# Optimization experiments

Measured on AMD Instinct MI355X. Metric: run time of the kernel, lower is better.

Reference implementation:

```python
import jax, jax.numpy as jnp
import numpy as np

B, G, K, H, NC = 128, 12000, 512, 64, 100
FP = 2048
ALPHA = 0.1
STEPS = 10

def setup_inputs() -> dict:
    key = jax.random.key(0)
    ks = jax.random.split(key, 10)
    ctl = jax.random.normal(ks[0], (B, G), jnp.float32)
    # drug targets: sparse binary indicator per gene
    drug_targets = (jax.random.uniform(ks[1], (B, G)) < 0.01).astype(jnp.float32)
    cell_idx = jax.random.randint(ks[2], (B,), 0, NC, dtype=jnp.int32)
    drug_fp = jax.random.normal(ks[3], (B, FP), jnp.float32)  # unused in forward
    # gene->module membership (sparse-ish binary), ensure each module non-empty via deg clamp in model
    M = (jax.random.uniform(ks[4], (G, K)) < 0.02).astype(jnp.float32)
    # row-stochastic module adjacency for stable diffusion
    Araw = jax.random.uniform(ks[5], (K, K), jnp.float32)
    A = Araw / jnp.sum(Araw, axis=1, keepdims=True)
    W_in = jax.random.normal(ks[6], (2, H), jnp.float32) * 0.5
    b_in = jnp.zeros((H,), jnp.float32)
    cell_emb = jax.random.normal(ks[7], (NC, H), jnp.float32) * 0.02
    W_out = jax.random.normal(ks[8], (H, 1), jnp.float32) * 0.1
    b_out = jnp.zeros((1,), jnp.float32)
    return {"ctl": ctl, "drug_targets": drug_targets, "cell_idx": cell_idx,
            "drug_fp": drug_fp, "M": M, "A": A, "W_in": W_in, "b_in": b_in,
            "cell_emb": cell_emb, "W_out": W_out, "b_out": b_out}

def reference(ctl, drug_targets, cell_idx, drug_fp, M, A, W_in, b_in, cell_emb, W_out, b_out):
    # module degree (clamped) as in __init__
    mod_deg = jnp.maximum(jnp.sum(M, axis=0), 1.0)            # [K]
    x_gene = jnp.stack([ctl, drug_targets], axis=-1)          # [B,G,2]
    x_mod = jnp.einsum('gk,bgh->bkh', M, x_gene) / mod_deg[None, :, None]  # [B,K,2]
    S = jax.nn.relu(x_mod @ W_in + b_in)                      # [B,K,H]
    # 10-step personalized-PageRank-style diffusion over modules
    def step(Z, _):
        Z = (1.0 - ALPHA) * jnp.einsum('bkh,kl->blh', Z, A) + ALPHA * S
        return Z, None
    Z, _ = jax.lax.scan(step, S, None, length=STEPS)          # [B,K,H]
    h_gene = jnp.einsum('gk,bkh->bgh', M, Z)                  # [B,G,H]
    h_gene = h_gene + cell_emb[cell_idx][:, None, :]          # add cell embedding
    y = (h_gene @ W_out + b_out)[..., 0]                      # [B,G]
    return y
```

## Files before the change

### kernel.cpp

```cpp
#include <hip/hip_runtime.h>

#define B_    128
#define G_    12000
#define GP    12288
#define K_    512
#define H_    64
#define NSEG  12
#define SEGG  1024
#define BKT   64

typedef __attribute__((ext_vector_type(8))) short bf16x8;
typedef __attribute__((ext_vector_type(4))) float f32x4;

__device__ __forceinline__ unsigned short f2bf(float x) {
    union { float f; unsigned u; } v; v.f = x;
    unsigned r = (v.u + 0x7FFFu + ((v.u >> 16) & 1u)) >> 16;
    return (unsigned short)r;
}
__device__ __forceinline__ float bf2f(unsigned short b) {
    union { float f; unsigned u; } v; v.u = ((unsigned)b) << 16;
    return v.f;
}

__device__ __forceinline__ void mm_body(int k0, int l0, float* __restrict__ sm,
        const float* __restrict__ Aop, const float* __restrict__ Bop,
        const float* __restrict__ Cop, const float* __restrict__ Dop,
        float alpha, float beta, float* __restrict__ O, float* __restrict__ O2) {
    float (*Xa)[68] = (float(*)[68])sm;
    float (*Xb)[36] = (float(*)[36])(sm + 2176);
    int tid = threadIdx.x;
    int kg = tid & 15, lg = tid >> 4;
    float acc[2][2] = {};
    for (int jj = 0; jj < K_; jj += 64) {
#pragma unroll
        for (int i = 0; i < 2; ++i) {
            int lin = tid + i * 256;
            int r = lin >> 4, c4 = lin & 15;
            *(float4*)&Xa[r][c4 * 4] =
                *(const float4*)&Aop[(size_t)(l0 + r) * K_ + jj + c4 * 4];
        }
#pragma unroll
        for (int i = 0; i < 2; ++i) {
            int lin = tid + i * 256;
            int r = lin >> 3, c4 = lin & 7;
            *(float4*)&Xb[r][c4 * 4] =
                *(const float4*)&Bop[(size_t)(jj + r) * K_ + k0 + c4 * 4];
        }
        __syncthreads();
#pragma unroll 8
        for (int j = 0; j < 64; ++j) {
            float xa0 = Xa[lg * 2][j], xa1 = Xa[lg * 2 + 1][j];
            float xb0 = Xb[j][kg * 2], xb1 = Xb[j][kg * 2 + 1];
            acc[0][0] = fmaf(xa0, xb0, acc[0][0]);
            acc[0][1] = fmaf(xa0, xb1, acc[0][1]);
            acc[1][0] = fmaf(xa1, xb0, acc[1][0]);
            acc[1][1] = fmaf(xa1, xb1, acc[1][1]);
        }
        __syncthreads();
    }
#pragma unroll
    for (int i = 0; i < 2; ++i) {
        size_t idx = (size_t)(l0 + lg * 2 + i) * K_ + k0 + kg * 2;
        float2 v;
        v.x = alpha * acc[i][0];
        v.y = alpha * acc[i][1];
        if (beta != 0.0f) {
            float2 cc = *(const float2*)&Cop[idx];
            v.x = fmaf(beta, cc.x, v.x);
            v.y = fmaf(beta, cc.y, v.y);
        }
        *(float2*)&O[idx] = v;
        if (O2) {
            float2 dd = *(const float2*)&Dop[idx];
            float2 w2; w2.x = v.x + dd.x; w2.y = v.y + dd.y;
            *(float2*)&O2[idx] = w2;
        }
    }
}

__global__ __launch_bounds__(256) void k_pre(
        const float* __restrict__ ctl, const float* __restrict__ dt,
        const float* __restrict__ M, const float* __restrict__ A,
        const int* __restrict__ cidx, const float* __restrict__ cemb,
        const float* __restrict__ W_out, const float* __restrict__ b_out,
        unsigned short* __restrict__ XpT, unsigned short* __restrict__ MTb,
        unsigned short* __restrict__ Mb,
        float* __restrict__ AT, float* __restrict__ U2,
        float* __restrict__ cvec) {
    __shared__ float t[32][33];
    int bid = blockIdx.x, tid = threadIdx.x;
    if (bid < 3072) {
        int p = bid / 12, chunk = bid % 12;
        int ch = p >> 7, b = p & 127;
        const float* src = (ch ? dt : ctl) + (size_t)b * G_;
        int g = chunk * 1024 + tid * 4;
        float x0 = 0.f, x1 = 0.f, x2 = 0.f, x3 = 0.f;
        if (g + 3 < G_) {
            float4 v = *(const float4*)&src[g];
            x0 = v.x; x1 = v.y; x2 = v.z; x3 = v.w;
        } else {
            if (g + 0 < G_) x0 = src[g + 0];
            if (g + 1 < G_) x1 = src[g + 1];
            if (g + 2 < G_) x2 = src[g + 2];
            if (g + 3 < G_) x3 = src[g + 3];
        }
        unsigned short h0 = f2bf(x0), h1 = f2bf(x1), h2 = f2bf(x2), h3 = f2bf(x3);
        ushort4 hv; hv.x = h0; hv.y = h1; hv.z = h2; hv.w = h3;
        *(ushort4*)&XpT[(size_t)p * GP + g] = hv;
        ushort4 lv;
        lv.x = f2bf(x0 - bf2f(h0)); lv.y = f2bf(x1 - bf2f(h1));
        lv.z = f2bf(x2 - bf2f(h2)); lv.w = f2bf(x3 - bf2f(h3));
        *(ushort4*)&XpT[(size_t)(p + 256) * GP + g] = lv;
    } else if (bid < 9216) {
        int id = bid - 3072;
        int gt = id % 384, kt = id / 384;
        int g0 = gt * 32, k0 = kt * 32;
        int tx = tid & 31, ty = tid >> 5;
#pragma unroll
        for (int j = 0; j < 4; ++j) {
            int g = g0 + ty + 8 * j;
            float v = (g < G_) ? M[(size_t)g * K_ + k0 + tx] : 0.0f;
            t[ty + 8 * j][tx] = v;
            Mb[(size_t)g * K_ + k0 + tx] = f2bf(v);
        }
        __syncthreads();
#pragma unroll
        for (int j = 0; j < 4; ++j)
            MTb[(size_t)(k0 + ty + 8 * j) * GP + g0 + tx] = f2bf(t[tx][ty + 8 * j]);
    } else if (bid < 9472) {
        int id = bid - 9216;
        int x0 = (id & 15) * 32, y0 = (id >> 4) * 32;
        int tx = tid & 31, ty = tid >> 5;
#pragma unroll
        for (int j = 0; j < 4; ++j)
            t[ty + 8 * j][tx] = A[(size_t)(y0 + ty + 8 * j) * K_ + x0 + tx];
        __syncthreads();
#pragma unroll
        for (int j = 0; j < 4; ++j) {
            int row = x0 + ty + 8 * j, col = y0 + tx;
            float v = t[tx][ty + 8 * j];
            AT[(size_t)row * K_ + col] = v;
            U2[(size_t)row * K_ + col] = 0.09f * v + (row == col ? 0.1f : 0.0f);
        }
    } else {
        if (tid < B_) {
            int ci = cidx[tid];
            float acc = b_out[0];
#pragma unroll 8
            for (int h = 0; h < H_; ++h)
                acc = fmaf(cemb[ci * H_ + h], W_out[h], acc);
            cvec[tid] = acc;
        }
    }
}

__global__ __launch_bounds__(256) void k_gemm(
        const unsigned short* __restrict__ MTb, const unsigned short* __restrict__ XpT,
        float* __restrict__ Cp,
        const float* __restrict__ AT, const float* __restrict__ U2,
        float* __restrict__ M2, float* __restrict__ Yop) {
    __shared__ __align__(16) char smraw[36864];
    int bid = blockIdx.x, tid = threadIdx.x;
    if (bid < 192) {
        unsigned short (*Al)[72] = (unsigned short(*)[72])smraw;
        unsigned short (*Bl)[72] = (unsigned short(*)[72])(smraw + 18432);
        int tile = bid & 15, seg = bid >> 4;
        int m0 = (tile & 3) * 128, n0 = (tile >> 2) * 128;
        size_t gbase = (size_t)seg * SEGG;
        int wid = tid >> 6, lane = tid & 63;
        int wm = (wid >> 1) * 64, wn = (wid & 1) * 64;
        int r16 = lane & 15, kg8 = (lane >> 4) * 8;
        int ld_row = tid >> 3, ld_c8 = (tid & 7) * 8;
        f32x4 acc[4][4] = {};
        for (int kk = 0; kk < SEGG; kk += BKT) {
#pragma unroll
            for (int i = 0; i < 4; ++i) {
                int r = ld_row + 32 * i;
                *(uint4*)&Al[r][ld_c8] =
                    *(const uint4*)&MTb[(size_t)(m0 + r) * GP + gbase + kk + ld_c8];
                *(uint4*)&Bl[r][ld_c8] =
                    *(const uint4*)&XpT[(size_t)(n0 + r) * GP + gbase + kk + ld_c8];
            }
            __syncthreads();
#pragma unroll
            for (int ks = 0; ks < 2; ++ks) {
                bf16x8 af[4], bf[4];
#pragma unroll
                for (int mi = 0; mi < 4; ++mi)
                    af[mi] = *(const bf16x8*)&Al[wm + mi * 16 + r16][ks * 32 + kg8];
#pragma unroll
                for (int ni = 0; ni < 4; ++ni)
                    bf[ni] = *(const bf16x8*)&Bl[wn + ni * 16 + r16][ks * 32 + kg8];
#pragma unroll
                for (int mi = 0; mi < 4; ++mi)
#pragma unroll
                    for (int ni = 0; ni < 4; ++ni)
                        acc[mi][ni] = __builtin_amdgcn_mfma_f32_16x16x32_bf16(
                            af[mi], bf[ni], acc[mi][ni], 0, 0, 0);
            }
            __syncthreads();
        }
        float* C = Cp + (size_t)seg * (K_ * K_);
        int cr = (lane >> 4) * 4, cc = lane & 15;
#pragma unroll
        for (int mi = 0; mi < 4; ++mi)
#pragma unroll
            for (int ni = 0; ni < 4; ++ni) {
                size_t rb = (size_t)(m0 + wm + mi * 16 + cr) * K_
                          + (n0 + wn + ni * 16 + cc);
#pragma unroll
                for (int r = 0; r < 4; ++r)
                    C[rb + (size_t)r * K_] = acc[mi][ni][r];
            }
    } else {
        int id = bid - 192;
        mm_body((id & 15) * 32, (id >> 4) * 32, (float*)smraw,
                AT, AT, nullptr, U2, 0.81f, 0.0f, M2, Yop);
    }
}

__global__ __launch_bounds__(256) void k_red(
        const float* __restrict__ Cp, const unsigned short* __restrict__ MTb,
        const float* __restrict__ W_in, const float* __restrict__ b_in,
        const float* __restrict__ W_out, float* __restrict__ sout,
        const float* __restrict__ M2, const float* __restrict__ U2,
        float* __restrict__ M4, float* __restrict__ U4) {
    __shared__ __align__(16) float sm[4480];
    int bid = blockIdx.x, tid = threadIdx.x;
    if (bid < 256) {
        int kloc = tid >> 7, b = tid & 127;
        int k = bid * 2 + kloc;
        int cnt = 0;
        const unsigned short* mrow = MTb + (size_t)k * GP;
#pragma unroll
        for (int i = 0; i < 12; ++i) {
            uint4 v = *(const uint4*)&mrow[i * 1024 + b * 8];
            cnt += ((v.x & 0xFFFFu) != 0) + ((v.x >> 16) != 0);
            cnt += ((v.y & 0xFFFFu) != 0) + ((v.y >> 16) != 0);
            cnt += ((v.z & 0xFFFFu) != 0) + ((v.z >> 16) != 0);
            cnt += ((v.w & 0xFFFFu) != 0) + ((v.w >> 16) != 0);
        }
#pragma unroll
        for (int off = 32; off; off >>= 1) cnt += __shfl_down(cnt, off, 64);
        __shared__ int dsum[4];
        __shared__ float degs[2];
        int wv = tid >> 6;
        if ((tid & 63) == 0) dsum[wv] = cnt;
        __syncthreads();
        if (tid < 2) degs[tid] = (float)(dsum[tid * 2] + dsum[tid * 2 + 1]);
        __syncthreads();
        float x0 = 0.f, x1 = 0.f;
        for (int s = 0; s < NSEG; ++s) {
            const float* Cb = Cp + (size_t)s * (K_ * K_) + (size_t)k * K_;
            x0 += Cb[b]       + Cb[256 + b];
            x1 += Cb[128 + b] + Cb[384 + b];
        }
        float inv = 1.0f / fmaxf(degs[kloc], 1.0f);
        x0 *= inv; x1 *= inv;
        float s = 0.f;
#pragma unroll 8
        for (int h = 0; h < H_; ++h) {
            float v = fmaf(x0, W_in[h], fmaf(x1, W_in[H_ + h], b_in[h]));
            v = fmaxf(v, 0.f);
            s = fmaf(v, W_out[h], s);
        }
        sout[k * B_ + b] = s;
    } else {
        int id = bid - 256;
        int t = id & 255;
        if (id < 256)
            mm_body((t & 15) * 32, (t >> 4) * 32, sm, M2, M2, nullptr, nullptr,
                    1.0f, 0.0f, M4, nullptr);
        else
            mm_body((t & 15) * 32, (t >> 4) * 32, sm, M2, U2, U2, nullptr,
                    1.0f, 1.0f, U4, nullptr);
    }
}

__global__ __launch_bounds__(256) void k_p3(
        const float* __restrict__ M4, const float* __restrict__ U4,
        float* __restrict__ M8, float* __restrict__ U8,
        const float* __restrict__ Yop, const float* __restrict__ sout,
        float* __restrict__ q) {
    __shared__ __align__(16) float sm[4480];
    int bid = blockIdx.x, tid = threadIdx.x;
    if (bid < 512) {
        int t = bid & 255;
        if (bid < 256)
            mm_body((t & 15) * 32, (t >> 4) * 32, sm, M4, M4, nullptr, nullptr,
                    1.0f, 0.0f, M8, nullptr);
        else
            mm_body((t & 15) * 32, (t >> 4) * 32, sm, M4, U4, U4, nullptr,
                    1.0f, 1.0f, U8, nullptr);
    } else {
        int l = bid - 512;
        float* Wr  = sm;
        float* red = sm + 512;
        if (tid < 128)
            ((float4*)Wr)[tid] = ((const float4*)&Yop[(size_t)l * K_])[tid];
        __syncthreads();
        int b = tid & 127, seg = tid >> 7;
        int kb = seg * 256;
        float a0 = 0.f, a1 = 0.f, a2 = 0.f, a3 = 0.f;
#pragma unroll 4
        for (int kk = 0; kk < 256; kk += 4) {
            int k = kb + kk;
            a0 = fmaf(Wr[k + 0], sout[(k + 0) * B_ + b], a0);
            a1 = fmaf(Wr[k + 1], sout[(k + 1) * B_ + b], a1);
            a2 = fmaf(Wr[k + 2], sout[(k + 2) * B_ + b], a2);
            a3 = fmaf(Wr[k + 3], sout[(k + 3) * B_ + b], a3);
        }
        red[seg * 128 + b] = (a0 + a1) + (a2 + a3);
        __syncthreads();
        if (tid < 128)
            q[l * B_ + b] = red[b] + red[128 + b];
    }
}

__global__ __launch_bounds__(1024) void k_zfin(
        const float* __restrict__ M8, const float* __restrict__ U8,
        const float* __restrict__ q, const float* __restrict__ sout,
        unsigned short* __restrict__ zbT) {
    __shared__ __align__(16) float Wr[4 * K_];
    __shared__ float red[8][2][128];
    int tid = threadIdx.x;
    int l0 = blockIdx.x * 2;
    if (tid < 256)
        ((float4*)Wr)[tid] = ((const float4*)&M8[(size_t)l0 * K_])[tid];
    else if (tid < 512)
        ((float4*)&Wr[2 * K_])[tid - 256] =
            ((const float4*)&U8[(size_t)l0 * K_])[tid - 256];
    __syncthreads();
    int b = tid & 127, seg = tid >> 7;
    int kb = seg * 64;
    float a0m = 0.f, a0u = 0.f, a1m = 0.f, a1u = 0.f;
#pragma unroll 8
    for (int kk = 0; kk < 64; ++kk) {
        int k = kb + kk;
        float qv = q[k * B_ + b];
        float sv = sout[k * B_ + b];
        a0m = fmaf(Wr[k], qv, a0m);
        a0u = fmaf(Wr[2 * K_ + k], sv, a0u);
        a1m = fmaf(Wr[K_ + k], qv, a1m);
        a1u = fmaf(Wr[3 * K_ + k], sv, a1u);
    }
    red[seg][0][b] = a0m + a0u;
    red[seg][1][b] = a1m + a1u;
    __syncthreads();
    if (tid < 256) {
        int row = tid >> 7, bb = tid & 127;
        float t = 0.f;
#pragma unroll
        for (int u = 0; u < 8; ++u) t += red[u][row][bb];
        unsigned short hi = f2bf(t);
        unsigned short lo = f2bf(t - bf2f(hi));
        zbT[(size_t)bb * (2 * K_) + (l0 + row)]      = hi;
        zbT[(size_t)bb * (2 * K_) + K_ + (l0 + row)] = lo;
    }
}

__global__ __launch_bounds__(256) void k_yg(
        const unsigned short* __restrict__ Mb, const unsigned short* __restrict__ zbT,
        const float* __restrict__ cvec, float* __restrict__ y) {
    __shared__ __align__(16) unsigned short Al[128][72];
    __shared__ __align__(16) unsigned short Bh[128][72];
    __shared__ __align__(16) unsigned short Bl2[128][72];
    int tid = threadIdx.x;
    int g0 = blockIdx.x * 128;
    int wid = tid >> 6, lane = tid & 63;
    int wm = (wid >> 1) * 64, wn = (wid & 1) * 64;
    int r16 = lane & 15, kg8 = (lane >> 4) * 8;
    int ld_row = tid >> 3, ld_c8 = (tid & 7) * 8;
    f32x4 acc[4][4] = {};
    for (int kk = 0; kk < K_; kk += BKT) {
#pragma unroll
        for (int i = 0; i < 4; ++i) {
            int r = ld_row + 32 * i;
            *(uint4*)&Al[r][ld_c8] =
                *(const uint4*)&Mb[(size_t)(g0 + r) * K_ + kk + ld_c8];
            *(uint4*)&Bh[r][ld_c8] =
                *(const uint4*)&zbT[(size_t)r * (2 * K_) + kk + ld_c8];
            *(uint4*)&Bl2[r][ld_c8] =
                *(const uint4*)&zbT[(size_t)r * (2 * K_) + K_ + kk + ld_c8];
        }
        __syncthreads();
#pragma unroll
        for (int ks = 0; ks < 2; ++ks) {
            bf16x8 af[4], bh[4], bl[4];
#pragma unroll
            for (int mi = 0; mi < 4; ++mi)
                af[mi] = *(const bf16x8*)&Al[wm + mi * 16 + r16][ks * 32 + kg8];
#pragma unroll
            for (int ni = 0; ni < 4; ++ni) {
                bh[ni] = *(const bf16x8*)&Bh[wn + ni * 16 + r16][ks * 32 + kg8];
                bl[ni] = *(const bf16x8*)&Bl2[wn + ni * 16 + r16][ks * 32 + kg8];
            }
#pragma unroll
            for (int mi = 0; mi < 4; ++mi)
#pragma unroll
                for (int ni = 0; ni < 4; ++ni) {
                    acc[mi][ni] = __builtin_amdgcn_mfma_f32_16x16x32_bf16(
                        af[mi], bh[ni], acc[mi][ni], 0, 0, 0);
                    acc[mi][ni] = __builtin_amdgcn_mfma_f32_16x16x32_bf16(
                        af[mi], bl[ni], acc[mi][ni], 0, 0, 0);
                }
        }
        __syncthreads();
    }
    int cr = (lane >> 4) * 4, cc = lane & 15;
#pragma unroll
    for (int ni = 0; ni < 4; ++ni) {
        int b = wn + ni * 16 + cc;
        float cv = cvec[b];
#pragma unroll
        for (int mi = 0; mi < 4; ++mi) {
            int g = g0 + wm + mi * 16 + cr;
            if (g < G_) {
                float4 o;
                o.x = acc[mi][ni][0] + cv;
                o.y = acc[mi][ni][1] + cv;
                o.z = acc[mi][ni][2] + cv;
                o.w = acc[mi][ni][3] + cv;
                *(float4*)&y[(size_t)b * G_ + g] = o;
            }
        }
    }
}

extern "C" void kernel_launch(void* const* d_in, const int* in_sizes, int n_in,
                              void* d_out, int out_size, void* d_ws, size_t ws_size,
                              hipStream_t stream) {
    const float* ctl   = (const float*)d_in[0];
    const float* dt    = (const float*)d_in[1];
    const int*   cidx  = (const int*)d_in[2];
    const float* M     = (const float*)d_in[4];
    const float* A     = (const float*)d_in[5];
    const float* W_in  = (const float*)d_in[6];
    const float* b_in  = (const float*)d_in[7];
    const float* cemb  = (const float*)d_in[8];
    const float* W_out = (const float*)d_in[9];
    const float* b_out = (const float*)d_in[10];
    float* y = (float*)d_out;

    char* ws = (char*)d_ws;
    size_t o = 0;
    auto take = [&](size_t bytes) { char* p = ws + o; o = (o + bytes + 255) & ~(size_t)255; return p; };
    unsigned short* XpT = (unsigned short*)take((size_t)512 * GP * 2);
    unsigned short* MTb = (unsigned short*)take((size_t)K_ * GP * 2);
    unsigned short* Mb  = (unsigned short*)take((size_t)GP * K_ * 2);
    unsigned short* zbT = (unsigned short*)take((size_t)B_ * 2 * K_ * 2);
    float* Cp   = (float*)take((size_t)NSEG * K_ * K_ * 4);
    float* cvec = (float*)take(B_ * 4);
    float* AT   = (float*)take((size_t)K_ * K_ * 4);
    float* U2   = (float*)take((size_t)K_ * K_ * 4);
    float* M2   = (float*)take((size_t)K_ * K_ * 4);
    float* Yop  = (float*)take((size_t)K_ * K_ * 4);
    float* M4   = (float*)take((size_t)K_ * K_ * 4);
    float* U4   = (float*)take((size_t)K_ * K_ * 4);
    float* M8   = (float*)take((size_t)K_ * K_ * 4);
    float* U8   = (float*)take((size_t)K_ * K_ * 4);
    float* sout = (float*)take((size_t)K_ * B_ * 4);
    float* q    = (float*)take((size_t)K_ * B_ * 4);
    (void)ws_size; (void)in_sizes; (void)n_in; (void)out_size;

    k_pre<<<9473, 256, 0, stream>>>(ctl, dt, M, A, cidx, cemb, W_out, b_out,
                                    XpT, MTb, Mb, AT, U2, cvec);
    k_gemm<<<448, 256, 0, stream>>>(MTb, XpT, Cp, AT, U2, M2, Yop);
    k_red<<<768, 256, 0, stream>>>(Cp, MTb, W_in, b_in, W_out, sout,
                                   M2, U2, M4, U4);
    k_p3<<<1024, 256, 0, stream>>>(M4, U4, M8, U8, Yop, sout, q);
    k_zfin<<<K_ / 2, 1024, 0, stream>>>(M8, U8, q, sout, zbT);
    k_yg<<<(G_ + 127) / 128, 256, 0, stream>>>(Mb, zbT, cvec, y);
}
```

Measured before the change: 110.8 us.

## Drop bf16 lo-residual split of inputs and fuse module degree count into transpose

Result: no change. 112.9 us (+1.8%).

```diff
diff --git a/kernel.cpp b/kernel.cpp
--- a/kernel.cpp
+++ b/kernel.cpp
@@ -5,8 +5,8 @@
 #define GP    12288
 #define K_    512
 #define H_    64
-#define NSEG  12
-#define SEGG  1024
+#define NSEG  24
+#define SEGG  512
 #define BKT   64
 
 typedef __attribute__((ext_vector_type(8))) short bf16x8;
@@ -84,10 +84,9 @@
         const int* __restrict__ cidx, const float* __restrict__ cemb,
         const float* __restrict__ W_out, const float* __restrict__ b_out,
         unsigned short* __restrict__ XpT, unsigned short* __restrict__ MTb,
-        unsigned short* __restrict__ Mb,
+        unsigned short* __restrict__ Mb, int* __restrict__ deg,
         float* __restrict__ AT, float* __restrict__ U2,
         float* __restrict__ cvec) {
-    __shared__ float t[32][33];
     int bid = blockIdx.x, tid = threadIdx.x;
     if (bid < 3072) {
         int p = bid / 12, chunk = bid % 12;
@@ -104,31 +103,37 @@
             if (g + 2 < G_) x2 = src[g + 2];
             if (g + 3 < G_) x3 = src[g + 3];
         }
-        unsigned short h0 = f2bf(x0), h1 = f2bf(x1), h2 = f2bf(x2), h3 = f2bf(x3);
-        ushort4 hv; hv.x = h0; hv.y = h1; hv.z = h2; hv.w = h3;
+        ushort4 hv;
+        hv.x = f2bf(x0); hv.y = f2bf(x1); hv.z = f2bf(x2); hv.w = f2bf(x3);
         *(ushort4*)&XpT[(size_t)p * GP + g] = hv;
-        ushort4 lv;
-        lv.x = f2bf(x0 - bf2f(h0)); lv.y = f2bf(x1 - bf2f(h1));
-        lv.z = f2bf(x2 - bf2f(h2)); lv.w = f2bf(x3 - bf2f(h3));
-        *(ushort4*)&XpT[(size_t)(p + 256) * GP + g] = lv;
-    } else if (bid < 9216) {
+    } else if (bid < 4608) {
+        __shared__ float t[64][65];
+        __shared__ int csum[4][64];
         int id = bid - 3072;
-        int gt = id % 384, kt = id / 384;
-        int g0 = gt * 32, k0 = kt * 32;
-        int tx = tid & 31, ty = tid >> 5;
-#pragma unroll
-        for (int j = 0; j < 4; ++j) {
-            int g = g0 + ty + 8 * j;
+        int gt = id % 192, kt = id / 192;
+        int g0 = gt * 64, k0 = kt * 64;
+        int tx = tid & 63, ty = tid >> 6;
+        int cnt = 0;
+#pragma unroll
+        for (int j = 0; j < 16; ++j) {
+            int g = g0 + ty + 4 * j;
             float v = (g < G_) ? M[(size_t)g * K_ + k0 + tx] : 0.0f;
-            t[ty + 8 * j][tx] = v;
+            t[ty + 4 * j][tx] = v;
             Mb[(size_t)g * K_ + k0 + tx] = f2bf(v);
-        }
-        __syncthreads();
-#pragma unroll
-        for (int j = 0; j < 4; ++j)
-            MTb[(size_t)(k0 + ty + 8 * j) * GP + g0 + tx] = f2bf(t[tx][ty + 8 * j]);
-    } else if (bid < 9472) {
-        int id = bid - 9216;
+            cnt += (v != 0.0f);
+        }
+        csum[ty][tx] = cnt;
+        __syncthreads();
+        if (ty == 0)
+            atomicAdd(&deg[k0 + tx],
+                      csum[0][tx] + csum[1][tx] + csum[2][tx] + csum[3][tx]);
+#pragma unroll
+        for (int j = 0; j < 16; ++j)
+            MTb[(size_t)(k0 + ty + 4 * j) * GP + g0 + tx] =
+                f2bf(t[tx][ty + 4 * j]);
+    } else if (bid < 4864) {
+        __shared__ float t[32][33];
+        int id = bid - 4608;
         int x0 = (id & 15) * 32, y0 = (id >> 4) * 32;
         int tx = tid & 31, ty = tid >> 5;
 #pragma unroll
@@ -164,7 +169,7 @@
     if (bid < 192) {
         unsigned short (*Al)[72] = (unsigned short(*)[72])smraw;
         unsigned short (*Bl)[72] = (unsigned short(*)[72])(smraw + 18432);
-        int tile = bid & 15, seg = bid >> 4;
+        int tile = bid & 7, seg = bid >> 3;
         int m0 = (tile & 3) * 128, n0 = (tile >> 2) * 128;
         size_t gbase = (size_t)seg * SEGG;
         int wid = tid >> 6, lane = tid & 63;
@@ -200,17 +205,17 @@
             }
             __syncthreads();
         }
-        float* C = Cp + (size_t)seg * (K_ * K_);
+        float* C = Cp + (size_t)seg * (K_ * 256);
         int cr = (lane >> 4) * 4, cc = lane & 15;
 #pragma unroll
         for (int mi = 0; mi < 4; ++mi)
 #pragma unroll
             for (int ni = 0; ni < 4; ++ni) {
-                size_t rb = (size_t)(m0 + wm + mi * 16 + cr) * K_
+                size_t rb = (size_t)(m0 + wm + mi * 16 + cr) * 256
                           + (n0 + wn + ni * 16 + cc);
 #pragma unroll
                 for (int r = 0; r < 4; ++r)
-                    C[rb + (size_t)r * K_] = acc[mi][ni][r];
+                    C[rb + (size_t)r * 256] = acc[mi][ni][r];
             }
     } else {
         int id = bid - 192;
@@ -220,7 +225,7 @@
 }
 
 __global__ __launch_bounds__(256) void k_red(
-        const float* __restrict__ Cp, const unsigned short* __restrict__ MTb,
+        const float* __restrict__ Cp, const int* __restrict__ deg,
         const float* __restrict__ W_in, const float* __restrict__ b_in,
         const float* __restrict__ W_out, float* __restrict__ sout,
         const float* __restrict__ M2, const float* __restrict__ U2,
@@ -230,32 +235,14 @@
     if (bid < 256) {
         int kloc = tid >> 7, b = tid & 127;
         int k = bid * 2 + kloc;
-        int cnt = 0;
-        const unsigned short* mrow = MTb + (size_t)k * GP;
-#pragma unroll
-        for (int i = 0; i < 12; ++i) {
-            uint4 v = *(const uint4*)&mrow[i * 1024 + b * 8];
-            cnt += ((v.x & 0xFFFFu) != 0) + ((v.x >> 16) != 0);
-            cnt += ((v.y & 0xFFFFu) != 0) + ((v.y >> 16) != 0);
-            cnt += ((v.z & 0xFFFFu) != 0) + ((v.z >> 16) != 0);
-            cnt += ((v.w & 0xFFFFu) != 0) + ((v.w >> 16) != 0);
-        }
-#pragma unroll
-        for (int off = 32; off; off >>= 1) cnt += __shfl_down(cnt, off, 64);
-        __shared__ int dsum[4];
-        __shared__ float degs[2];
-        int wv = tid >> 6;
-        if ((tid & 63) == 0) dsum[wv] = cnt;
-        __syncthreads();
-        if (tid < 2) degs[tid] = (float)(dsum[tid * 2] + dsum[tid * 2 + 1]);
-        __syncthreads();
         float x0 = 0.f, x1 = 0.f;
+#pragma unroll 4
         for (int s = 0; s < NSEG; ++s) {
-            const float* Cb = Cp + (size_t)s * (K_ * K_) + (size_t)k * K_;
-            x0 += Cb[b]       + Cb[256 + b];
-            x1 += Cb[128 + b] + Cb[384 + b];
-        }
-        float inv = 1.0f / fmaxf(degs[kloc], 1.0f);
+            const float* Cb = Cp + (size_t)s * (K_ * 256) + (size_t)k * 256;
+            x0 += Cb[b];
+            x1 += Cb[128 + b];
+        }
+        float inv = 1.0f / fmaxf((float)deg[k], 1.0f);
         x0 *= inv; x1 *= inv;
         float s = 0.f;
 #pragma unroll 8
@@ -445,11 +432,12 @@
     char* ws = (char*)d_ws;
     size_t o = 0;
     auto take = [&](size_t bytes) { char* p = ws + o; o = (o + bytes + 255) & ~(size_t)255; return p; };
-    unsigned short* XpT = (unsigned short*)take((size_t)512 * GP * 2);
+    unsigned short* XpT = (unsigned short*)take((size_t)256 * GP * 2);
     unsigned short* MTb = (unsigned short*)take((size_t)K_ * GP * 2);
     unsigned short* Mb  = (unsigned short*)take((size_t)GP * K_ * 2);
     unsigned short* zbT = (unsigned short*)take((size_t)B_ * 2 * K_ * 2);
-    float* Cp   = (float*)take((size_t)NSEG * K_ * K_ * 4);
+    float* Cp   = (float*)take((size_t)NSEG * K_ * 256 * 4);
+    int*   deg  = (int*)  take(K_ * 4);
     float* cvec = (float*)take(B_ * 4);
     float* AT   = (float*)take((size_t)K_ * K_ * 4);
     float* U2   = (float*)take((size_t)K_ * K_ * 4);
@@ -463,10 +451,11 @@
     float* q    = (float*)take((size_t)K_ * B_ * 4);
     (void)ws_size; (void)in_sizes; (void)n_in; (void)out_size;
 
-    k_pre<<<9473, 256, 0, stream>>>(ctl, dt, M, A, cidx, cemb, W_out, b_out,
-                                    XpT, MTb, Mb, AT, U2, cvec);
+    hipMemsetAsync(deg, 0, K_ * 4, stream);
+    k_pre<<<4865, 256, 0, stream>>>(ctl, dt, M, A, cidx, cemb, W_out, b_out,
+                                    XpT, MTb, Mb, deg, AT, U2, cvec);
     k_gemm<<<448, 256, 0, stream>>>(MTb, XpT, Cp, AT, U2, M2, Yop);
-    k_red<<<768, 256, 0, stream>>>(Cp, MTb, W_in, b_in, W_out, sout,
+    k_red<<<768, 256, 0, stream>>>(Cp, deg, W_in, b_in, W_out, sout,
                                    M2, U2, M4, U4);
     k_p3<<<1024, 256, 0, stream>>>(M4, U4, M8, U8, Yop, sout, q);
     k_zfin<<<K_ / 2, 1024, 0, stream>>>(M8, U8, q, sout, zbT);
```
